# Performance work log

Hardware: AMD Instinct MI355X
Metric: run time of the kernel (lower is better)

Reference implementation:

```python
import jax, jax.numpy as jnp
import numpy as np

D_IN, D_OUT, H, L = 18, 2, 128, 2  # from load_pretrained config; bidirectional


def _uniform(key, shape, scale):
    return jax.random.uniform(key, shape, jnp.float32, -scale, scale)


def setup_inputs() -> dict:
    key = jax.random.key(0)
    ks = jax.random.split(key, 32)
    B, T = 64, 2048
    s = 1.0 / np.sqrt(H)
    inp = {"x": jax.random.normal(ks[0], (B, T, D_IN), jnp.float32)}
    i = 1
    for l in range(L):
        d_in_l = D_IN if l == 0 else 2 * H
        for suf in ("", "r"):
            inp[f"w_ih_l{l}{suf}"] = _uniform(ks[i], (3 * H, d_in_l), s); i += 1
            inp[f"w_hh_l{l}{suf}"] = _uniform(ks[i], (3 * H, H), s); i += 1
            inp[f"b_ih_l{l}{suf}"] = _uniform(ks[i], (3 * H,), s); i += 1
            inp[f"b_hh_l{l}{suf}"] = _uniform(ks[i], (3 * H,), s); i += 1
    inp["fc_w"] = _uniform(ks[i], (D_OUT, 2 * H), 1.0 / np.sqrt(2 * H)); i += 1
    inp["fc_b"] = _uniform(ks[i], (D_OUT,), 1.0 / np.sqrt(2 * H))
    return inp


def gru_dir(x, w_ih, w_hh, b_ih, b_hh, reverse):
    # x: [B,T,Din] -> [B,T,H], PyTorch GRU gate math (r,z,n ordering)
    B, T, _ = x.shape
    xg = jnp.einsum('btd,gd->btg', x, w_ih) + b_ih  # [B,T,3H], batched GEMM once
    if reverse:
        xg = xg[:, ::-1]
    def step(h, xt):
        gh = h @ w_hh.T + b_hh
        xr, xz, xn = jnp.split(xt, 3, axis=-1)
        hr, hz, hn = jnp.split(gh, 3, axis=-1)
        r = jax.nn.sigmoid(xr + hr)
        z = jax.nn.sigmoid(xz + hz)
        n = jnp.tanh(xn + r * hn)
        h_new = (1.0 - z) * n + z * h
        return h_new, h_new
    h0 = jnp.zeros((B, H), x.dtype)
    _, ys = jax.lax.scan(step, h0, jnp.swapaxes(xg, 0, 1))  # scan over time
    ys = jnp.swapaxes(ys, 0, 1)
    if reverse:
        ys = ys[:, ::-1]
    return ys


def gru_forward(x, params):
    h = x
    for l in range(L):
        fwd = gru_dir(h, params[f"w_ih_l{l}"], params[f"w_hh_l{l}"],
                      params[f"b_ih_l{l}"], params[f"b_hh_l{l}"], False)
        bwd = gru_dir(h, params[f"w_ih_l{l}r"], params[f"w_hh_l{l}r"],
                      params[f"b_ih_l{l}r"], params[f"b_hh_l{l}r"], True)
        h = jnp.concatenate([fwd, bwd], axis=-1)  # [B,T,2H]; dropout off (eval)
    return h


def reference(x, w_ih_l0, w_hh_l0, b_ih_l0, b_hh_l0,
              w_ih_l0r, w_hh_l0r, b_ih_l0r, b_hh_l0r,
              w_ih_l1, w_hh_l1, b_ih_l1, b_hh_l1,
              w_ih_l1r, w_hh_l1r, b_ih_l1r, b_hh_l1r,
              fc_w, fc_b):
    params = dict(w_ih_l0=w_ih_l0, w_hh_l0=w_hh_l0, b_ih_l0=b_ih_l0, b_hh_l0=b_hh_l0,
                  w_ih_l0r=w_ih_l0r, w_hh_l0r=w_hh_l0r, b_ih_l0r=b_ih_l0r, b_hh_l0r=b_hh_l0r,
                  w_ih_l1=w_ih_l1, w_hh_l1=w_hh_l1, b_ih_l1=b_ih_l1, b_hh_l1=b_hh_l1,
                  w_ih_l1r=w_ih_l1r, w_hh_l1r=w_hh_l1r, b_ih_l1r=b_ih_l1r, b_hh_l1r=b_hh_l1r)
    h = gru_forward(x, params)
    return jnp.einsum('bth,oh->bto', h, fc_w) + fc_b  # [B,T,D_OUT]
```

## Files before the change

kernel.cpp:

```cpp
#include <hip/hip_runtime.h>
#include <hip/hip_bf16.h>

#define B_   64
#define T_   2048
#define H_   128
#define G_   384
#define D0_  18
#define WIN  4
#define RING 8
#define NW   (T_ / WIN)

typedef __hip_bfloat16 bf16;
typedef __attribute__((ext_vector_type(4))) float f32x4;
typedef __attribute__((ext_vector_type(8))) short s16x8;

#define LOG2E  1.4426950408889634f
#define NEGL2E (-1.4426950408889634f)
#define TWOL2E (2.8853900817779268f)

__device__ __forceinline__ short f2bs(float v) {
    bf16 b = __float2bfloat16(v);
    return *reinterpret_cast<short*>(&b);
}
__device__ __forceinline__ unsigned short f2bu(float v) {
    bf16 b = __float2bfloat16(v);
    return *reinterpret_cast<unsigned short*>(&b);
}
__device__ __forceinline__ uint2 pk_bf16x4(float a, float b, float c, float d) {
    uint2 r;
    asm("v_cvt_pk_bf16_f32 %0, %1, %2" : "=v"(r.x) : "v"(a), "v"(b));
    asm("v_cvt_pk_bf16_f32 %0, %1, %2" : "=v"(r.y) : "v"(c), "v"(d));
    return r;
}
#define MFMA16(A, B, C) __builtin_amdgcn_mfma_f32_16x16x32_bf16((A), (B), (C), 0, 0, 0)

__device__ __forceinline__ void step_sync() {
    __asm__ volatile("s_waitcnt lgkmcnt(0)" ::: "memory");
    __builtin_amdgcn_s_barrier();
    __asm__ volatile("" ::: "memory");
}

__device__ __forceinline__ float gru_update(float yr, float yz, float aN,
                                            float aX, float h) {
    const float Er = __builtin_amdgcn_exp2f(yr);
    const float rg = __builtin_amdgcn_rcpf(1.0f + Er);
    const float En = __builtin_amdgcn_exp2f(fmaf(rg, aN, aX));
    const float Ez = __builtin_amdgcn_exp2f(yz);
    const float p  = fmaf(En, Ez, -Ez);
    const float q2 = fmaf(h, En, h);
    const float t1 = Ez + 1.0f;
    const float dn = fmaf(En, t1, t1);
    return (p + q2) * __builtin_amdgcn_rcpf(dn);
}


__global__ __launch_bounds__(512) void gru_l0_mfma(
    const float* __restrict__ x,
    const float* __restrict__ wih_f, const float* __restrict__ whh_f,
    const float* __restrict__ bih_f, const float* __restrict__ bhh_f,
    const float* __restrict__ wih_r, const float* __restrict__ whh_r,
    const float* __restrict__ bih_r, const float* __restrict__ bhh_r,
    bf16* __restrict__ l0h)
{
    __shared__ __align__(16) bf16 hring[RING][2048];
    __shared__ __align__(16) bf16 xbuf[2][WIN][512];

    const int bx   = blockIdx.x;
    const int dir  = bx >> 2;
    const int bg   = bx & 3;
    const int b0   = bg * 16;
    const int tid  = threadIdx.x;
    const int lane = tid & 63;
    const int wv   = tid >> 6;
    const int col  = lane & 15;
    const int quad = lane >> 4;

    const float* Wih = dir ? wih_r : wih_f;
    const float* Whh = dir ? whh_r : whh_f;
    const float* Bih = dir ? bih_r : bih_f;
    const float* Bhh = dir ? bhh_r : bhh_f;

    const float GSC[3] = {NEGL2E, NEGL2E, TWOL2E};

    s16x8 wfr[3][4], wxf[3];
    #pragma unroll
    for (int g = 0; g < 3; ++g) {
        const float sc = GSC[g];
        const float* wrow = Whh + (size_t)(g * H_ + wv * 16 + col) * H_;
        #pragma unroll
        for (int kt = 0; kt < 4; ++kt) {
            const float* p = wrow + kt * 32 + quad * 8;
            s16x8 f;
            #pragma unroll
            for (int i = 0; i < 8; ++i) f[i] = f2bs(p[i] * sc);
            wfr[g][kt] = f;
        }
        const float* xrow = Wih + (size_t)(g * H_ + wv * 16 + col) * D0_;
        s16x8 fx;
        #pragma unroll
        for (int i = 0; i < 8; ++i) {
            const int k = quad * 8 + i;
            fx[i] = (k < D0_) ? f2bs(xrow[k] * sc) : (short)0;
        }
        wxf[g] = fx;
    }
    f32x4 sR, sZ, sX, sN;
    #pragma unroll
    for (int r = 0; r < 4; ++r) {
        const int j = wv * 16 + quad * 4 + r;
        sR[r] = (Bih[j]        + Bhh[j])      * NEGL2E;
        sZ[r] = (Bih[H_ + j]   + Bhh[H_ + j]) * NEGL2E;
        sX[r] = Bih[2*H_ + j]  * TWOL2E;
        sN[r] = Bhh[2*H_ + j]  * TWOL2E;
    }

    const int wkt   = wv >> 1;
    const int wl    = (((wv << 1) + (quad >> 1)) & 3) * 16 + col;
    const int woff  = wkt * 512 + wl * 8 + (quad & 1) * 4;

    for (int i = tid; i < 2048; i += 512) hring[0][i] = __float2bfloat16(0.0f);
    #pragma unroll
    for (int k = 0; k < 4; ++k) {
        const int i = tid + k * 512;
        const int si = i >> 9, rem = i & 511;
        const int m = (rem >> 5) & 15, c = rem & 31;
        const int t = dir ? (T_ - 1 - si) : si;
        const float v = (c < D0_) ? x[((size_t)(b0 + m) * T_ + t) * D0_ + c] : 0.0f;
        xbuf[0][si][((c >> 3) * 16 + m) * 8 + (c & 7)] = __float2bfloat16(v);
    }
    __syncthreads();

    float hprev[4] = {0.f, 0.f, 0.f, 0.f};
    float xv[4];

    for (int w = 0; w < NW; ++w) {
        const int par = w & 1;
        s16x8 axf[WIN];
        #pragma unroll
        for (int si = 0; si < WIN; ++si)
            axf[si] = *(const s16x8*)&xbuf[par][si][lane * 8];

        #pragma unroll
        for (int si = 0; si < WIN; ++si) {
            const int s  = w * WIN + si;
            const int rb = s & (RING - 1);
            const int wb = (s + 1) & (RING - 1);

            s16x8 hfr[4];
            #pragma unroll
            for (int kt = 0; kt < 4; ++kt)
                hfr[kt] = *(const s16x8*)&hring[rb][kt * 512 + lane * 8];

            f32x4 aR = MFMA16(wxf[0], axf[si], sR);
            f32x4 aZ = MFMA16(wxf[1], axf[si], sZ);
            f32x4 aX = MFMA16(wxf[2], axf[si], sX);
            f32x4 aN = sN;
            #pragma unroll
            for (int kt = 0; kt < 4; ++kt) {
                aR = MFMA16(wfr[0][kt], hfr[kt], aR);
                aZ = MFMA16(wfr[1][kt], hfr[kt], aZ);
                aN = MFMA16(wfr[2][kt], hfr[kt], aN);
            }

            if (si == 1 && w > 0) {
                #pragma unroll
                for (int k = 0; k < 2; ++k) {
                    const int c  = tid + k * 512;
                    const int dt = c >> 8, m = (c >> 4) & 15, jo = c & 15;
                    const int fs = (w - 1) * WIN + dt;
                    const int t  = dir ? (T_ - 1 - fs) : fs;
                    const uint4 v = *(const uint4*)
                        &hring[(fs + 1) & (RING - 1)][(jo >> 2) * 512 + ((jo & 3) * 16 + m) * 8];
                    *(uint4*)(l0h + ((size_t)(b0 + m) * T_ + t) * 256 + dir * H_ + jo * 8) = v;
                }
            }

            if (si == 0 && w + 1 < NW) {
                #pragma unroll
                for (int k = 0; k < 4; ++k) {
                    const int i = tid + k * 512;
                    const int sj = i >> 9, rem = i & 511;
                    const int m = (rem >> 5) & 15, c = rem & 31;
                    const int s2 = (w + 1) * WIN + sj;
                    const int t2 = dir ? (T_ - 1 - s2) : s2;
                    xv[k] = (c < D0_) ? x[((size_t)(b0 + m) * T_ + t2) * D0_ + c] : 0.0f;
                }
            }

            float hn4[4];
            #pragma unroll
            for (int r = 0; r < 4; ++r) {
                const float hn = gru_update(aR[r], aZ[r], aN[r], aX[r], hprev[r]);
                hprev[r] = hn;
                hn4[r] = hn;
            }
            *(uint2*)&hring[wb][woff] = pk_bf16x4(hn4[0], hn4[1], hn4[2], hn4[3]);

            if (si == 3 && w + 1 < NW) {
                #pragma unroll
                for (int k = 0; k < 4; ++k) {
                    const int i = tid + k * 512;
                    const int sj = i >> 9, rem = i & 511;
                    const int m = (rem >> 5) & 15, c = rem & 31;
                    xbuf[par ^ 1][sj][((c >> 3) * 16 + m) * 8 + (c & 7)] =
                        __float2bfloat16(xv[k]);
                }
            }
            step_sync();
        }
    }
    #pragma unroll
    for (int k = 0; k < 2; ++k) {
        const int c  = tid + k * 512;
        const int dt = c >> 8, m = (c >> 4) & 15, jo = c & 15;
        const int fs = (NW - 1) * WIN + dt;
        const int t  = dir ? (T_ - 1 - fs) : fs;
        const uint4 v = *(const uint4*)
            &hring[(fs + 1) & (RING - 1)][(jo >> 2) * 512 + ((jo & 3) * 16 + m) * 8];
        *(uint4*)(l0h + ((size_t)(b0 + m) * T_ + t) * 256 + dir * H_ + jo * 8) = v;
    }
}

__global__ __launch_bounds__(256, 2) void xg_gemm_mfma(
    const bf16* __restrict__ A,
    const float* __restrict__ w_f, const float* __restrict__ w_r,
    const float* __restrict__ bi_f, const float* __restrict__ bi_r,
    const float* __restrict__ bh_f, const float* __restrict__ bh_r,
    bf16* __restrict__ xg_f, bf16* __restrict__ xg_r)
{
    __shared__ short As[128 * 40];
    __shared__ short Ws[128 * 40];
    __shared__ float Bias_s[128];

    const int dir  = blockIdx.z;
    const float* W   = dir ? w_r : w_f;
    const float* bi  = dir ? bi_r : bi_f;
    const float* bh  = dir ? bh_r : bh_f;
    bf16* xg         = dir ? xg_r : xg_f;

    const int tid  = threadIdx.x;
    const int lane = tid & 63;
    const int wv   = tid >> 6;
    const int col  = lane & 15;
    const int quad = lane >> 4;
    const int n0   = blockIdx.x * 128;
    const int g    = blockIdx.y;
    const int m0   = g * 128;

    const float sc = (g < 2) ? NEGL2E : TWOL2E;

    if (tid < 128) {
        const int n = m0 + tid;
        Bias_s[tid] = (bi[n] + ((n < 2 * H_) ? bh[n] : 0.0f)) * sc;
    }

    f32x4 acc[2][8];
    #pragma unroll
    for (int mt = 0; mt < 2; ++mt)
        #pragma unroll
        for (int nt = 0; nt < 8; ++nt) acc[mt][nt] = (f32x4){0.f, 0.f, 0.f, 0.f};

    for (int k0 = 0; k0 < 256; k0 += 32) {
        #pragma unroll
        for (int i = 0; i < 2; ++i) {
            const int c = tid + i * 256;
            const int row = c >> 2, q4 = c & 3;
            *(uint4*)&As[row * 40 + q4 * 8] =
                *(const uint4*)(A + (size_t)(n0 + row) * 256 + k0 + q4 * 8);
        }
        #pragma unroll
        for (int i = 0; i < 4; ++i) {
            const int c = tid + i * 256;
            const int row = c >> 3, q = c & 7;
            const float4 v = *(const float4*)(W + (size_t)(m0 + row) * 256 + k0 + q * 4);
            ushort4 u;
            u.x = f2bu(v.x * sc); u.y = f2bu(v.y * sc);
            u.z = f2bu(v.z * sc); u.w = f2bu(v.w * sc);
            *(ushort4*)&Ws[row * 40 + q * 4] = u;
        }
        __syncthreads();

        s16x8 wfr[2], hfr[8];
        #pragma unroll
        for (int mt = 0; mt < 2; ++mt)
            wfr[mt] = *(const s16x8*)&Ws[(wv * 32 + mt * 16 + col) * 40 + quad * 8];
        #pragma unroll
        for (int nt = 0; nt < 8; ++nt)
            hfr[nt] = *(const s16x8*)&As[(nt * 16 + col) * 40 + quad * 8];

        #pragma unroll
        for (int mt = 0; mt < 2; ++mt)
            #pragma unroll
            for (int nt = 0; nt < 8; ++nt)
                acc[mt][nt] = MFMA16(wfr[mt], hfr[nt], acc[mt][nt]);
        __syncthreads();
    }

    const int batch = n0 >> 11;
    const int bg = batch >> 4, cm = batch & 15;
    #pragma unroll
    for (int mt = 0; mt < 2; ++mt) {
        const int jt = wv * 2 + mt;
        float bv[4];
        #pragma unroll
        for (int r = 0; r < 4; ++r)
            bv[r] = Bias_s[wv * 32 + mt * 16 + quad * 4 + r];
        #pragma unroll
        for (int nt = 0; nt < 8; ++nt) {
            const int t = (n0 & 2047) + nt * 16 + col;
            uint2 o;
            o.x = (unsigned)f2bu(acc[mt][nt][0] + bv[0]) |
                  ((unsigned)f2bu(acc[mt][nt][1] + bv[1]) << 16);
            o.y = (unsigned)f2bu(acc[mt][nt][2] + bv[2]) |
                  ((unsigned)f2bu(acc[mt][nt][3] + bv[3]) << 16);
            const size_t idx = ((((size_t)bg * T_ + t) * 3 + g) * 8 + jt) * 64
                             + quad * 16 + cm;
            ((uint2*)xg)[idx] = o;
        }
    }
}

__global__ __launch_bounds__(512) void gru_l1_mfma(
    const bf16* __restrict__ xg_f, const bf16* __restrict__ xg_r,
    const float* __restrict__ whh_f, const float* __restrict__ bhh_f,
    const float* __restrict__ whh_r, const float* __restrict__ bhh_r,
    bf16* __restrict__ l1h, int fixed_dir)
{
    __shared__ __align__(16) bf16 hring[RING][2048];

    const int bx   = blockIdx.x;
    const int dir  = (fixed_dir >= 0) ? fixed_dir : (bx >> 2);
    const int bg   = bx & 3;
    const int b0   = bg * 16;
    const int tid  = threadIdx.x;
    const int lane = tid & 63;
    const int wv   = tid >> 6;
    const int col  = lane & 15;
    const int quad = lane >> 4;

    const bf16*  XG  = dir ? xg_r : xg_f;
    const float* Whh = dir ? whh_r : whh_f;
    const float* Bhh = dir ? bhh_r : bhh_f;

    const float GSC[3] = {NEGL2E, NEGL2E, TWOL2E};

    s16x8 wfr[3][4];
    #pragma unroll
    for (int g = 0; g < 3; ++g) {
        const float sc = GSC[g];
        const float* wrow = Whh + (size_t)(g * H_ + wv * 16 + col) * H_;
        #pragma unroll
        for (int kt = 0; kt < 4; ++kt) {
            const float* p = wrow + kt * 32 + quad * 8;
            s16x8 f;
            #pragma unroll
            for (int i = 0; i < 8; ++i) f[i] = f2bs(p[i] * sc);
            wfr[g][kt] = f;
        }
    }
    f32x4 sN;
    #pragma unroll
    for (int r = 0; r < 4; ++r)
        sN[r] = Bhh[2*H_ + wv * 16 + quad * 4 + r] * TWOL2E;

    const int wkt  = wv >> 1;
    const int wl   = (((wv << 1) + (quad >> 1)) & 3) * 16 + col;
    const int woff = wkt * 512 + wl * 8 + (quad & 1) * 4;

    for (int i = tid; i < 2048; i += 512) hring[0][i] = __float2bfloat16(0.0f);

    const uint2* xgb = (const uint2*)XG + ((size_t)bg * T_) * 3 * 8 * 64;
    const int lidx = wv * 64 + lane;

    uint2 xcur[WIN][3], xnxt[WIN][3];
    #pragma unroll
    for (int si = 0; si < WIN; ++si) {
        const int t = dir ? (T_ - 1 - si) : si;
        #pragma unroll
        for (int g = 0; g < 3; ++g)
            xcur[si][g] = xgb[((size_t)t * 3 + g) * 512 + lidx];
    }
    __syncthreads();

    float hprev[4] = {0.f, 0.f, 0.f, 0.f};

    for (int w = 0; w < NW; ++w) {
        #pragma unroll
        for (int si = 0; si < WIN; ++si) {
            const int s  = w * WIN + si;
            const int rb = s & (RING - 1);
            const int wb = (s + 1) & (RING - 1);

            s16x8 hfr[4];
            #pragma unroll
            for (int kt = 0; kt < 4; ++kt)
                hfr[kt] = *(const s16x8*)&hring[rb][kt * 512 + lane * 8];

            const uint2 xr2 = xcur[si][0], xz2 = xcur[si][1], xn2 = xcur[si][2];
            const f32x4 seedR = (f32x4){
                __uint_as_float(xr2.x << 16), __uint_as_float(xr2.x & 0xffff0000u),
                __uint_as_float(xr2.y << 16), __uint_as_float(xr2.y & 0xffff0000u)};
            const f32x4 seedZ = (f32x4){
                __uint_as_float(xz2.x << 16), __uint_as_float(xz2.x & 0xffff0000u),
                __uint_as_float(xz2.y << 16), __uint_as_float(xz2.y & 0xffff0000u)};
            const float xnf[4] = {
                __uint_as_float(xn2.x << 16), __uint_as_float(xn2.x & 0xffff0000u),
                __uint_as_float(xn2.y << 16), __uint_as_float(xn2.y & 0xffff0000u)};

            f32x4 aR = seedR, aZ = seedZ, aN = sN;
            #pragma unroll
            for (int kt = 0; kt < 4; ++kt) {
                aR = MFMA16(wfr[0][kt], hfr[kt], aR);
                aZ = MFMA16(wfr[1][kt], hfr[kt], aZ);
                aN = MFMA16(wfr[2][kt], hfr[kt], aN);
            }

            if (si == 1 && w > 0) {
                #pragma unroll
                for (int k = 0; k < 2; ++k) {
                    const int c  = tid + k * 512;
                    const int dt = c >> 8, m = (c >> 4) & 15, jo = c & 15;
                    const int fs = (w - 1) * WIN + dt;
                    const int t  = dir ? (T_ - 1 - fs) : fs;
                    const uint4 v = *(const uint4*)
                        &hring[(fs + 1) & (RING - 1)][(jo >> 2) * 512 + ((jo & 3) * 16 + m) * 8];
                    *(uint4*)(l1h + ((size_t)(b0 + m) * T_ + t) * 256 + dir * H_ + jo * 8) = v;
                }
            }

            if (si == 0 && w + 1 < NW) {
                #pragma unroll
                for (int sj = 0; sj < WIN; ++sj) {
                    const int s2 = (w + 1) * WIN + sj;
                    const int t2 = dir ? (T_ - 1 - s2) : s2;
                    #pragma unroll
                    for (int g = 0; g < 3; ++g)
                        xnxt[sj][g] = xgb[((size_t)t2 * 3 + g) * 512 + lidx];
                }
            }

            float hn4[4];
            #pragma unroll
            for (int r = 0; r < 4; ++r) {
                const float hn = gru_update(aR[r], aZ[r], aN[r], xnf[r], hprev[r]);
                hprev[r] = hn;
                hn4[r] = hn;
            }
            *(uint2*)&hring[wb][woff] = pk_bf16x4(hn4[0], hn4[1], hn4[2], hn4[3]);

            step_sync();
        }

        #pragma unroll
        for (int si = 0; si < WIN; ++si) {
            xcur[si][0] = xnxt[si][0];
            xcur[si][1] = xnxt[si][1];
            xcur[si][2] = xnxt[si][2];
        }
    }
    #pragma unroll
    for (int k = 0; k < 2; ++k) {
        const int c  = tid + k * 512;
        const int dt = c >> 8, m = (c >> 4) & 15, jo = c & 15;
        const int fs = (NW - 1) * WIN + dt;
        const int t  = dir ? (T_ - 1 - fs) : fs;
        const uint4 v = *(const uint4*)
            &hring[(fs + 1) & (RING - 1)][(jo >> 2) * 512 + ((jo & 3) * 16 + m) * 8];
        *(uint4*)(l1h + ((size_t)(b0 + m) * T_ + t) * 256 + dir * H_ + jo * 8) = v;
    }
}

__global__ __launch_bounds__(256, 2) void fc_kernel(
    const bf16* __restrict__ h, const float* __restrict__ fcw,
    const float* __restrict__ fcb, float* __restrict__ out)
{
    __shared__ float w0[256], w1[256];
    const int tid = threadIdx.x;
    w0[tid] = fcw[tid];
    w1[tid] = fcw[256 + tid];
    __syncthreads();

    const size_t bt = (size_t)blockIdx.x * 256 + tid;
    const bf16* hp = h + bt * 256;
    float s0 = fcb[0], s1 = fcb[1];
    #pragma unroll 4
    for (int k8 = 0; k8 < 32; ++k8) {
        const uint4 u = *(const uint4*)(hp + k8 * 8);
        const unsigned uu[4] = {u.x, u.y, u.z, u.w};
        #pragma unroll
        for (int p = 0; p < 4; ++p) {
            const float v0 = __uint_as_float(uu[p] << 16);
            const float v1 = __uint_as_float(uu[p] & 0xffff0000u);
            const int k = k8 * 8 + p * 2;
            s0 = fmaf(w0[k], v0, s0);     s1 = fmaf(w1[k], v0, s1);
            s0 = fmaf(w0[k + 1], v1, s0); s1 = fmaf(w1[k + 1], v1, s1);
        }
    }
    out[bt * 2]     = s0;
    out[bt * 2 + 1] = s1;
}

extern "C" void kernel_launch(void* const* d_in, const int* in_sizes, int n_in,
                              void* d_out, int out_size, void* d_ws, size_t ws_size,
                              hipStream_t stream)
{
    if (n_in < 19) return;
    const float* x     = (const float*)d_in[0];
    const float* wih0  = (const float*)d_in[1];
    const float* whh0  = (const float*)d_in[2];
    const float* bih0  = (const float*)d_in[3];
    const float* bhh0  = (const float*)d_in[4];
    const float* wih0r = (const float*)d_in[5];
    const float* whh0r = (const float*)d_in[6];
    const float* bih0r = (const float*)d_in[7];
    const float* bhh0r = (const float*)d_in[8];
    const float* wih1  = (const float*)d_in[9];
    const float* whh1  = (const float*)d_in[10];
    const float* bih1  = (const float*)d_in[11];
    const float* bhh1  = (const float*)d_in[12];
    const float* wih1r = (const float*)d_in[13];
    const float* whh1r = (const float*)d_in[14];
    const float* bih1r = (const float*)d_in[15];
    const float* bhh1r = (const float*)d_in[16];
    const float* fcw   = (const float*)d_in[17];
    const float* fcb   = (const float*)d_in[18];
    float* out = (float*)d_out;

    const size_t nBT  = (size_t)B_ * T_;
    const size_t hh_b = nBT * 2 * H_ * sizeof(bf16);
    const size_t xg_b = nBT * G_ * sizeof(bf16);
    const size_t xg_el = nBT * G_;

    if (ws_size >= hh_b + 2 * xg_b) {
        bf16* l0h = (bf16*)d_ws;
        bf16* xgf = (bf16*)((char*)d_ws + hh_b);
        bf16* xgr = xgf + xg_el;

        gru_l0_mfma<<<dim3(8), dim3(512), 0, stream>>>(
            x, wih0, whh0, bih0, bhh0, wih0r, whh0r, bih0r, bhh0r, l0h);
        xg_gemm_mfma<<<dim3(1024, 3, 2), dim3(256), 0, stream>>>(
            l0h, wih1, wih1r, bih1, bih1r, bhh1, bhh1r, xgf, xgr);
        gru_l1_mfma<<<dim3(8), dim3(512), 0, stream>>>(
            xgf, xgr, whh1, bhh1, whh1r, bhh1r, l0h, -1);
        fc_kernel<<<dim3((int)(nBT / 256)), dim3(256), 0, stream>>>(l0h, fcw, fcb, out);
    } else if (ws_size >= 2 * hh_b + xg_b) {
        bf16* l0h = (bf16*)d_ws;
        bf16* xg  = (bf16*)((char*)d_ws + hh_b);
        bf16* l1h = (bf16*)((char*)d_ws + hh_b + xg_b);

        gru_l0_mfma<<<dim3(8), dim3(512), 0, stream>>>(
            x, wih0, whh0, bih0, bhh0, wih0r, whh0r, bih0r, bhh0r, l0h);
        xg_gemm_mfma<<<dim3(1024, 3, 1), dim3(256), 0, stream>>>(
            l0h, wih1, wih1, bih1, bih1, bhh1, bhh1, xg, xg);
        gru_l1_mfma<<<dim3(4), dim3(512), 0, stream>>>(
            xg, xg, whh1, bhh1, whh1r, bhh1r, l1h, 0);
        xg_gemm_mfma<<<dim3(1024, 3, 1), dim3(256), 0, stream>>>(
            l0h, wih1r, wih1r, bih1r, bih1r, bhh1r, bhh1r, xg, xg);
        gru_l1_mfma<<<dim3(4), dim3(512), 0, stream>>>(
            xg, xg, whh1, bhh1, whh1r, bhh1r, l1h, 1);
        fc_kernel<<<dim3((int)(nBT / 256)), dim3(256), 0, stream>>>(l1h, fcw, fcb, out);
    }
}
```

Baseline: 2.592 ms.

## Precompute layer-0 input gates with a GEMM and reuse the layer-1 recurrence kernel

Removes the dedicated layer-0 recurrent kernel, which did the small x·W_ih projection with MFMAs inside the serial time loop. A new parallel GEMM kernel now precomputes the layer-0 input gate pre-activations into the xg buffer, and the existing layer-1 recurrent kernel is reused for layer 0. This takes the x loading and input-projection MFMAs off the latency-critical sequential path. The cost is an extra kernel launch plus a write and read of the xg buffer through global memory.

```diff
diff --git a/kernel.cpp b/kernel.cpp
--- a/kernel.cpp
+++ b/kernel.cpp
@@ -53,272 +53,6 @@
     return (p + q2) * __builtin_amdgcn_rcpf(dn);
 }
 
-
-__global__ __launch_bounds__(512) void gru_l0_mfma(
-    const float* __restrict__ x,
-    const float* __restrict__ wih_f, const float* __restrict__ whh_f,
-    const float* __restrict__ bih_f, const float* __restrict__ bhh_f,
-    const float* __restrict__ wih_r, const float* __restrict__ whh_r,
-    const float* __restrict__ bih_r, const float* __restrict__ bhh_r,
-    bf16* __restrict__ l0h)
-{
-    __shared__ __align__(16) bf16 hring[RING][2048];
-    __shared__ __align__(16) bf16 xbuf[2][WIN][512];
-
-    const int bx   = blockIdx.x;
-    const int dir  = bx >> 2;
-    const int bg   = bx & 3;
-    const int b0   = bg * 16;
-    const int tid  = threadIdx.x;
-    const int lane = tid & 63;
-    const int wv   = tid >> 6;
-    const int col  = lane & 15;
-    const int quad = lane >> 4;
-
-    const float* Wih = dir ? wih_r : wih_f;
-    const float* Whh = dir ? whh_r : whh_f;
-    const float* Bih = dir ? bih_r : bih_f;
-    const float* Bhh = dir ? bhh_r : bhh_f;
-
-    const float GSC[3] = {NEGL2E, NEGL2E, TWOL2E};
-
-    s16x8 wfr[3][4], wxf[3];
-    #pragma unroll
-    for (int g = 0; g < 3; ++g) {
-        const float sc = GSC[g];
-        const float* wrow = Whh + (size_t)(g * H_ + wv * 16 + col) * H_;
-        #pragma unroll
-        for (int kt = 0; kt < 4; ++kt) {
-            const float* p = wrow + kt * 32 + quad * 8;
-            s16x8 f;
-            #pragma unroll
-            for (int i = 0; i < 8; ++i) f[i] = f2bs(p[i] * sc);
-            wfr[g][kt] = f;
-        }
-        const float* xrow = Wih + (size_t)(g * H_ + wv * 16 + col) * D0_;
-        s16x8 fx;
-        #pragma unroll
-        for (int i = 0; i < 8; ++i) {
-            const int k = quad * 8 + i;
-            fx[i] = (k < D0_) ? f2bs(xrow[k] * sc) : (short)0;
-        }
-        wxf[g] = fx;
-    }
-    f32x4 sR, sZ, sX, sN;
-    #pragma unroll
-    for (int r = 0; r < 4; ++r) {
-        const int j = wv * 16 + quad * 4 + r;
-        sR[r] = (Bih[j]        + Bhh[j])      * NEGL2E;
-        sZ[r] = (Bih[H_ + j]   + Bhh[H_ + j]) * NEGL2E;
-        sX[r] = Bih[2*H_ + j]  * TWOL2E;
-        sN[r] = Bhh[2*H_ + j]  * TWOL2E;
-    }
-
-    const int wkt   = wv >> 1;
-    const int wl    = (((wv << 1) + (quad >> 1)) & 3) * 16 + col;
-    const int woff  = wkt * 512 + wl * 8 + (quad & 1) * 4;
-
-    for (int i = tid; i < 2048; i += 512) hring[0][i] = __float2bfloat16(0.0f);
-    #pragma unroll
-    for (int k = 0; k < 4; ++k) {
-        const int i = tid + k * 512;
-        const int si = i >> 9, rem = i & 511;
-        const int m = (rem >> 5) & 15, c = rem & 31;
-        const int t = dir ? (T_ - 1 - si) : si;
-        const float v = (c < D0_) ? x[((size_t)(b0 + m) * T_ + t) * D0_ + c] : 0.0f;
-        xbuf[0][si][((c >> 3) * 16 + m) * 8 + (c & 7)] = __float2bfloat16(v);
-    }
-    __syncthreads();
-
-    float hprev[4] = {0.f, 0.f, 0.f, 0.f};
-    float xv[4];
-
-    for (int w = 0; w < NW; ++w) {
-        const int par = w & 1;
-        s16x8 axf[WIN];
-        #pragma unroll
-        for (int si = 0; si < WIN; ++si)
-            axf[si] = *(const s16x8*)&xbuf[par][si][lane * 8];
-
-        #pragma unroll
-        for (int si = 0; si < WIN; ++si) {
-            const int s  = w * WIN + si;
-            const int rb = s & (RING - 1);
-            const int wb = (s + 1) & (RING - 1);
-
-            s16x8 hfr[4];
-            #pragma unroll
-            for (int kt = 0; kt < 4; ++kt)
-                hfr[kt] = *(const s16x8*)&hring[rb][kt * 512 + lane * 8];
-
-            f32x4 aR = MFMA16(wxf[0], axf[si], sR);
-            f32x4 aZ = MFMA16(wxf[1], axf[si], sZ);
-            f32x4 aX = MFMA16(wxf[2], axf[si], sX);
-            f32x4 aN = sN;
-            #pragma unroll
-            for (int kt = 0; kt < 4; ++kt) {
-                aR = MFMA16(wfr[0][kt], hfr[kt], aR);
-                aZ = MFMA16(wfr[1][kt], hfr[kt], aZ);
-                aN = MFMA16(wfr[2][kt], hfr[kt], aN);
-            }
-
-            if (si == 1 && w > 0) {
-                #pragma unroll
-                for (int k = 0; k < 2; ++k) {
-                    const int c  = tid + k * 512;
-                    const int dt = c >> 8, m = (c >> 4) & 15, jo = c & 15;
-                    const int fs = (w - 1) * WIN + dt;
-                    const int t  = dir ? (T_ - 1 - fs) : fs;
-                    const uint4 v = *(const uint4*)
-                        &hring[(fs + 1) & (RING - 1)][(jo >> 2) * 512 + ((jo & 3) * 16 + m) * 8];
-                    *(uint4*)(l0h + ((size_t)(b0 + m) * T_ + t) * 256 + dir * H_ + jo * 8) = v;
-                }
-            }
-
-            if (si == 0 && w + 1 < NW) {
-                #pragma unroll
-                for (int k = 0; k < 4; ++k) {
-                    const int i = tid + k * 512;
-                    const int sj = i >> 9, rem = i & 511;
-                    const int m = (rem >> 5) & 15, c = rem & 31;
-                    const int s2 = (w + 1) * WIN + sj;
-                    const int t2 = dir ? (T_ - 1 - s2) : s2;
-                    xv[k] = (c < D0_) ? x[((size_t)(b0 + m) * T_ + t2) * D0_ + c] : 0.0f;
-                }
-            }
-
-            float hn4[4];
-            #pragma unroll
-            for (int r = 0; r < 4; ++r) {
-                const float hn = gru_update(aR[r], aZ[r], aN[r], aX[r], hprev[r]);
-                hprev[r] = hn;
-                hn4[r] = hn;
-            }
-            *(uint2*)&hring[wb][woff] = pk_bf16x4(hn4[0], hn4[1], hn4[2], hn4[3]);
-
-            if (si == 3 && w + 1 < NW) {
-                #pragma unroll
-                for (int k = 0; k < 4; ++k) {
-                    const int i = tid + k * 512;
-                    const int sj = i >> 9, rem = i & 511;
-                    const int m = (rem >> 5) & 15, c = rem & 31;
-                    xbuf[par ^ 1][sj][((c >> 3) * 16 + m) * 8 + (c & 7)] =
-                        __float2bfloat16(xv[k]);
-                }
-            }
-            step_sync();
-        }
-    }
-    #pragma unroll
-    for (int k = 0; k < 2; ++k) {
-        const int c  = tid + k * 512;
-        const int dt = c >> 8, m = (c >> 4) & 15, jo = c & 15;
-        const int fs = (NW - 1) * WIN + dt;
-        const int t  = dir ? (T_ - 1 - fs) : fs;
-        const uint4 v = *(const uint4*)
-            &hring[(fs + 1) & (RING - 1)][(jo >> 2) * 512 + ((jo & 3) * 16 + m) * 8];
-        *(uint4*)(l0h + ((size_t)(b0 + m) * T_ + t) * 256 + dir * H_ + jo * 8) = v;
-    }
-}
-
-__global__ __launch_bounds__(256, 2) void xg_gemm_mfma(
-    const bf16* __restrict__ A,
-    const float* __restrict__ w_f, const float* __restrict__ w_r,
-    const float* __restrict__ bi_f, const float* __restrict__ bi_r,
-    const float* __restrict__ bh_f, const float* __restrict__ bh_r,
-    bf16* __restrict__ xg_f, bf16* __restrict__ xg_r)
-{
-    __shared__ short As[128 * 40];
-    __shared__ short Ws[128 * 40];
-    __shared__ float Bias_s[128];
-
-    const int dir  = blockIdx.z;
-    const float* W   = dir ? w_r : w_f;
-    const float* bi  = dir ? bi_r : bi_f;
-    const float* bh  = dir ? bh_r : bh_f;
-    bf16* xg         = dir ? xg_r : xg_f;
-
-    const int tid  = threadIdx.x;
-    const int lane = tid & 63;
-    const int wv   = tid >> 6;
-    const int col  = lane & 15;
-    const int quad = lane >> 4;
-    const int n0   = blockIdx.x * 128;
-    const int g    = blockIdx.y;
-    const int m0   = g * 128;
-
-    const float sc = (g < 2) ? NEGL2E : TWOL2E;
-
-    if (tid < 128) {
-        const int n = m0 + tid;
-        Bias_s[tid] = (bi[n] + ((n < 2 * H_) ? bh[n] : 0.0f)) * sc;
-    }
-
-    f32x4 acc[2][8];
-    #pragma unroll
-    for (int mt = 0; mt < 2; ++mt)
-        #pragma unroll
-        for (int nt = 0; nt < 8; ++nt) acc[mt][nt] = (f32x4){0.f, 0.f, 0.f, 0.f};
-
-    for (int k0 = 0; k0 < 256; k0 += 32) {
-        #pragma unroll
-        for (int i = 0; i < 2; ++i) {
-            const int c = tid + i * 256;
-            const int row = c >> 2, q4 = c & 3;
-            *(uint4*)&As[row * 40 + q4 * 8] =
-                *(const uint4*)(A + (size_t)(n0 + row) * 256 + k0 + q4 * 8);
-        }
-        #pragma unroll
-        for (int i = 0; i < 4; ++i) {
-            const int c = tid + i * 256;
-            const int row = c >> 3, q = c & 7;
-            const float4 v = *(const float4*)(W + (size_t)(m0 + row) * 256 + k0 + q * 4);
-            ushort4 u;
-            u.x = f2bu(v.x * sc); u.y = f2bu(v.y * sc);
-            u.z = f2bu(v.z * sc); u.w = f2bu(v.w * sc);
-            *(ushort4*)&Ws[row * 40 + q * 4] = u;
-        }
-        __syncthreads();
-
-        s16x8 wfr[2], hfr[8];
-        #pragma unroll
-        for (int mt = 0; mt < 2; ++mt)
-            wfr[mt] = *(const s16x8*)&Ws[(wv * 32 + mt * 16 + col) * 40 + quad * 8];
-        #pragma unroll
-        for (int nt = 0; nt < 8; ++nt)
-            hfr[nt] = *(const s16x8*)&As[(nt * 16 + col) * 40 + quad * 8];
-
-        #pragma unroll
-        for (int mt = 0; mt < 2; ++mt)
-            #pragma unroll
-            for (int nt = 0; nt < 8; ++nt)
-                acc[mt][nt] = MFMA16(wfr[mt], hfr[nt], acc[mt][nt]);
-        __syncthreads();
-    }
-
-    const int batch = n0 >> 11;
-    const int bg = batch >> 4, cm = batch & 15;
-    #pragma unroll
-    for (int mt = 0; mt < 2; ++mt) {
-        const int jt = wv * 2 + mt;
-        float bv[4];
-        #pragma unroll
-        for (int r = 0; r < 4; ++r)
-            bv[r] = Bias_s[wv * 32 + mt * 16 + quad * 4 + r];
-        #pragma unroll
-        for (int nt = 0; nt < 8; ++nt) {
-            const int t = (n0 & 2047) + nt * 16 + col;
-            uint2 o;
-            o.x = (unsigned)f2bu(acc[mt][nt][0] + bv[0]) |
-                  ((unsigned)f2bu(acc[mt][nt][1] + bv[1]) << 16);
-            o.y = (unsigned)f2bu(acc[mt][nt][2] + bv[2]) |
-                  ((unsigned)f2bu(acc[mt][nt][3] + bv[3]) << 16);
-            const size_t idx = ((((size_t)bg * T_ + t) * 3 + g) * 8 + jt) * 64
-                             + quad * 16 + cm;
-            ((uint2*)xg)[idx] = o;
-        }
-    }
-}
 
 __global__ __launch_bounds__(512) void gru_l1_mfma(
     const bf16* __restrict__ xg_f, const bf16* __restrict__ xg_r,
@@ -467,6 +201,196 @@
         const uint4 v = *(const uint4*)
             &hring[(fs + 1) & (RING - 1)][(jo >> 2) * 512 + ((jo & 3) * 16 + m) * 8];
         *(uint4*)(l1h + ((size_t)(b0 + m) * T_ + t) * 256 + dir * H_ + jo * 8) = v;
+    }
+}
+
+__global__ __launch_bounds__(256, 2) void xg_gemm_mfma(
+    const bf16* __restrict__ A,
+    const float* __restrict__ w_f, const float* __restrict__ w_r,
+    const float* __restrict__ bi_f, const float* __restrict__ bi_r,
+    const float* __restrict__ bh_f, const float* __restrict__ bh_r,
+    bf16* __restrict__ xg_f, bf16* __restrict__ xg_r)
+{
+    __shared__ short As[128 * 40];
+    __shared__ short Ws[128 * 40];
+    __shared__ float Bias_s[128];
+
+    const int dir  = blockIdx.z;
+    const float* W   = dir ? w_r : w_f;
+    const float* bi  = dir ? bi_r : bi_f;
+    const float* bh  = dir ? bh_r : bh_f;
+    bf16* xg         = dir ? xg_r : xg_f;
+
+    const int tid  = threadIdx.x;
+    const int lane = tid & 63;
+    const int wv   = tid >> 6;
+    const int col  = lane & 15;
+    const int quad = lane >> 4;
+    const int n0   = blockIdx.x * 128;
+    const int g    = blockIdx.y;
+    const int m0   = g * 128;
+
+    const float sc = (g < 2) ? NEGL2E : TWOL2E;
+    const f32x4 z4 = {0.f, 0.f, 0.f, 0.f};
+
+    if (tid < 128) {
+        const int n = m0 + tid;
+        Bias_s[tid] = (bi[n] + ((n < 2 * H_) ? bh[n] : 0.0f)) * sc;
+    }
+
+    f32x4 acc[2][8];
+    #pragma unroll
+    for (int mt = 0; mt < 2; ++mt)
+        #pragma unroll
+        for (int nt = 0; nt < 8; ++nt) acc[mt][nt] = z4;
+
+    for (int k0 = 0; k0 < 256; k0 += 32) {
+        #pragma unroll
+        for (int i = 0; i < 2; ++i) {
+            const int c = tid + i * 256;
+            const int row = c >> 2, q4 = c & 3;
+            *(uint4*)&As[row * 40 + q4 * 8] =
+                *(const uint4*)(A + (size_t)(n0 + row) * 256 + k0 + q4 * 8);
+        }
+        #pragma unroll
+        for (int i = 0; i < 4; ++i) {
+            const int c = tid + i * 256;
+            const int row = c >> 3, q = c & 7;
+            const float4 v = *(const float4*)(W + (size_t)(m0 + row) * 256 + k0 + q * 4);
+            ushort4 u;
+            u.x = f2bu(v.x * sc); u.y = f2bu(v.y * sc);
+            u.z = f2bu(v.z * sc); u.w = f2bu(v.w * sc);
+            *(ushort4*)&Ws[row * 40 + q * 4] = u;
+        }
+        __syncthreads();
+
+        s16x8 wfr[2], hfr[8];
+        #pragma unroll
+        for (int mt = 0; mt < 2; ++mt)
+            wfr[mt] = *(const s16x8*)&Ws[(wv * 32 + mt * 16 + col) * 40 + quad * 8];
+        #pragma unroll
+        for (int nt = 0; nt < 8; ++nt)
+            hfr[nt] = *(const s16x8*)&As[(nt * 16 + col) * 40 + quad * 8];
+
+        #pragma unroll
+        for (int mt = 0; mt < 2; ++mt)
+            #pragma unroll
+            for (int nt = 0; nt < 8; ++nt)
+                acc[mt][nt] = MFMA16(wfr[mt], hfr[nt], acc[mt][nt]);
+        __syncthreads();
+    }
+
+    const int batch = n0 >> 11;
+    const int bg = batch >> 4, cm = batch & 15;
+    #pragma unroll
+    for (int mt = 0; mt < 2; ++mt) {
+        const int jt = wv * 2 + mt;
+        float bv[4];
+        #pragma unroll
+        for (int r = 0; r < 4; ++r)
+            bv[r] = Bias_s[wv * 32 + mt * 16 + quad * 4 + r];
+        #pragma unroll
+        for (int nt = 0; nt < 8; ++nt) {
+            const int t = (n0 & 2047) + nt * 16 + col;
+            uint2 o;
+            o.x = (unsigned)f2bu(acc[mt][nt][0] + bv[0]) |
+                  ((unsigned)f2bu(acc[mt][nt][1] + bv[1]) << 16);
+            o.y = (unsigned)f2bu(acc[mt][nt][2] + bv[2]) |
+                  ((unsigned)f2bu(acc[mt][nt][3] + bv[3]) << 16);
+            const size_t idx = ((((size_t)bg * T_ + t) * 3 + g) * 8 + jt) * 64
+                             + quad * 16 + cm;
+            ((uint2*)xg)[idx] = o;
+        }
+    }
+}
+
+__global__ __launch_bounds__(256, 2) void xg0_gemm_mfma(
+    const float* __restrict__ x,
+    const float* __restrict__ w_f, const float* __restrict__ w_r,
+    const float* __restrict__ bi_f, const float* __restrict__ bi_r,
+    const float* __restrict__ bh_f, const float* __restrict__ bh_r,
+    bf16* __restrict__ xg_f, bf16* __restrict__ xg_r)
+{
+    __shared__ short As[128 * 40];
+    __shared__ short Ws[128 * 40];
+    __shared__ float Bias_s[128];
+
+    const int dir  = blockIdx.z;
+    const float* W   = dir ? w_r : w_f;
+    const float* bi  = dir ? bi_r : bi_f;
+    const float* bh  = dir ? bh_r : bh_f;
+    bf16* xg         = dir ? xg_r : xg_f;
+
+    const int tid  = threadIdx.x;
+    const int lane = tid & 63;
+    const int wv   = tid >> 6;
+    const int col  = lane & 15;
+    const int quad = lane >> 4;
+    const int n0   = blockIdx.x * 128;
+    const int g    = blockIdx.y;
+    const int m0   = g * 128;
+
+    const float sc = (g < 2) ? NEGL2E : TWOL2E;
+    const f32x4 z4 = {0.f, 0.f, 0.f, 0.f};
+
+    if (tid < 128) {
+        const int n = m0 + tid;
+        Bias_s[tid] = (bi[n] + ((n < 2 * H_) ? bh[n] : 0.0f)) * sc;
+    }
+
+    for (int i = tid; i < 128 * 40 / 2; i += 256) {
+        ((unsigned*)As)[i] = 0u;
+        ((unsigned*)Ws)[i] = 0u;
+    }
+    __syncthreads();
+
+    const float* xb = x + (size_t)n0 * D0_;
+    for (int i = tid; i < 128 * D0_; i += 256) {
+        const int row = i / D0_, k = i - row * D0_;
+        As[row * 40 + k] = f2bs(xb[i]);
+    }
+    for (int i = tid; i < 128 * D0_; i += 256) {
+        const int row = i / D0_, k = i - row * D0_;
+        Ws[row * 40 + k] = f2bs(W[(size_t)(m0 + row) * D0_ + k] * sc);
+    }
+    __syncthreads();
+
+    s16x8 wfr[2], hfr[8];
+    #pragma unroll
+    for (int mt = 0; mt < 2; ++mt)
+        wfr[mt] = *(const s16x8*)&Ws[(wv * 32 + mt * 16 + col) * 40 + quad * 8];
+    #pragma unroll
+    for (int nt = 0; nt < 8; ++nt)
+        hfr[nt] = *(const s16x8*)&As[(nt * 16 + col) * 40 + quad * 8];
+
+    f32x4 acc[2][8];
+    #pragma unroll
+    for (int mt = 0; mt < 2; ++mt)
+        #pragma unroll
+        for (int nt = 0; nt < 8; ++nt)
+            acc[mt][nt] = MFMA16(wfr[mt], hfr[nt], z4);
+
+    const int batch = n0 >> 11;
+    const int bg = batch >> 4, cm = batch & 15;
+    #pragma unroll
+    for (int mt = 0; mt < 2; ++mt) {
+        const int jt = wv * 2 + mt;
+        float bv[4];
+        #pragma unroll
+        for (int r = 0; r < 4; ++r)
+            bv[r] = Bias_s[wv * 32 + mt * 16 + quad * 4 + r];
+        #pragma unroll
+        for (int nt = 0; nt < 8; ++nt) {
+            const int t = (n0 & 2047) + nt * 16 + col;
+            uint2 o;
+            o.x = (unsigned)f2bu(acc[mt][nt][0] + bv[0]) |
+                  ((unsigned)f2bu(acc[mt][nt][1] + bv[1]) << 16);
+            o.y = (unsigned)f2bu(acc[mt][nt][2] + bv[2]) |
+                  ((unsigned)f2bu(acc[mt][nt][3] + bv[3]) << 16);
+            const size_t idx = ((((size_t)bg * T_ + t) * 3 + g) * 8 + jt) * 64
+                             + quad * 16 + cm;
+            ((uint2*)xg)[idx] = o;
+        }
     }
 }
 
@@ -536,8 +460,10 @@
         bf16* xgf = (bf16*)((char*)d_ws + hh_b);
         bf16* xgr = xgf + xg_el;
 
-        gru_l0_mfma<<<dim3(8), dim3(512), 0, stream>>>(
-            x, wih0, whh0, bih0, bhh0, wih0r, whh0r, bih0r, bhh0r, l0h);
+        xg0_gemm_mfma<<<dim3(1024, 3, 2), dim3(256), 0, stream>>>(
+            x, wih0, wih0r, bih0, bih0r, bhh0, bhh0r, xgf, xgr);
+        gru_l1_mfma<<<dim3(8), dim3(512), 0, stream>>>(
+            xgf, xgr, whh0, bhh0, whh0r, bhh0r, l0h, -1);
         xg_gemm_mfma<<<dim3(1024, 3, 2), dim3(256), 0, stream>>>(
             l0h, wih1, wih1r, bih1, bih1r, bhh1, bhh1r, xgf, xgr);
         gru_l1_mfma<<<dim3(8), dim3(512), 0, stream>>>(
@@ -548,8 +474,14 @@
         bf16* xg  = (bf16*)((char*)d_ws + hh_b);
         bf16* l1h = (bf16*)((char*)d_ws + hh_b + xg_b);
 
-        gru_l0_mfma<<<dim3(8), dim3(512), 0, stream>>>(
-            x, wih0, whh0, bih0, bhh0, wih0r, whh0r, bih0r, bhh0r, l0h);
+        xg0_gemm_mfma<<<dim3(1024, 3, 1), dim3(256), 0, stream>>>(
+            x, wih0, wih0, bih0, bih0, bhh0, bhh0, xg, xg);
+        gru_l1_mfma<<<dim3(4), dim3(512), 0, stream>>>(
+            xg, xg, whh0, bhh0, whh0r, bhh0r, l0h, 0);
+        xg0_gemm_mfma<<<dim3(1024, 3, 1), dim3(256), 0, stream>>>(
+            x, wih0r, wih0r, bih0r, bih0r, bhh0r, bhh0r, xg, xg);
+        gru_l1_mfma<<<dim3(4), dim3(512), 0, stream>>>(
+            xg, xg, whh0, bhh0, whh0r, bhh0r, l0h, 1);
         xg_gemm_mfma<<<dim3(1024, 3, 1), dim3(256), 0, stream>>>(
             l0h, wih1, wih1, bih1, bih1, bhh1, bhh1, xg, xg);
         gru_l1_mfma<<<dim3(4), dim3(512), 0, stream>>>(
```

After: 2.751 ms. 6.1% more time.

## Fuse layer-1 input projection into recurrent GRU kernel with LDS prefetch

Applied to the files above, without the earlier changes.

Removes the separate xg_gemm kernel and its large bf16 gate buffer. The layer-1 recurrent kernel now keeps W_ih fragments in registers and computes the input projection per timestep with extra MFMAs. The l0h rows are streamed into a 4-slot LDS ring three steps ahead via global_load_lds. This cuts a launch and the xg write/read traffic, but adds 24 MFMAs per step to the serial critical path of an 8-block kernel and raises register pressure.

```diff
diff --git a/kernel.cpp b/kernel.cpp
--- a/kernel.cpp
+++ b/kernel.cpp
@@ -38,6 +38,12 @@
     __asm__ volatile("s_waitcnt lgkmcnt(0)" ::: "memory");
     __builtin_amdgcn_s_barrier();
     __asm__ volatile("" ::: "memory");
+}
+
+__device__ __forceinline__ void gload_lds16(const bf16* g, bf16* l) {
+    __builtin_amdgcn_global_load_lds(
+        (const __attribute__((address_space(1))) unsigned*)(const void*)g,
+        (__attribute__((address_space(3))) unsigned*)(void*)l, 16, 0, 0);
 }
 
 __device__ __forceinline__ float gru_update(float yr, float yz, float aN,
@@ -221,115 +227,19 @@
     }
 }
 
-__global__ __launch_bounds__(256, 2) void xg_gemm_mfma(
-    const bf16* __restrict__ A,
-    const float* __restrict__ w_f, const float* __restrict__ w_r,
-    const float* __restrict__ bi_f, const float* __restrict__ bi_r,
-    const float* __restrict__ bh_f, const float* __restrict__ bh_r,
-    bf16* __restrict__ xg_f, bf16* __restrict__ xg_r)
-{
-    __shared__ short As[128 * 40];
-    __shared__ short Ws[128 * 40];
-    __shared__ float Bias_s[128];
-
-    const int dir  = blockIdx.z;
-    const float* W   = dir ? w_r : w_f;
-    const float* bi  = dir ? bi_r : bi_f;
-    const float* bh  = dir ? bh_r : bh_f;
-    bf16* xg         = dir ? xg_r : xg_f;
-
-    const int tid  = threadIdx.x;
-    const int lane = tid & 63;
-    const int wv   = tid >> 6;
-    const int col  = lane & 15;
-    const int quad = lane >> 4;
-    const int n0   = blockIdx.x * 128;
-    const int g    = blockIdx.y;
-    const int m0   = g * 128;
-
-    const float sc = (g < 2) ? NEGL2E : TWOL2E;
-
-    if (tid < 128) {
-        const int n = m0 + tid;
-        Bias_s[tid] = (bi[n] + ((n < 2 * H_) ? bh[n] : 0.0f)) * sc;
-    }
-
-    f32x4 acc[2][8];
-    #pragma unroll
-    for (int mt = 0; mt < 2; ++mt)
-        #pragma unroll
-        for (int nt = 0; nt < 8; ++nt) acc[mt][nt] = (f32x4){0.f, 0.f, 0.f, 0.f};
-
-    for (int k0 = 0; k0 < 256; k0 += 32) {
-        #pragma unroll
-        for (int i = 0; i < 2; ++i) {
-            const int c = tid + i * 256;
-            const int row = c >> 2, q4 = c & 3;
-            *(uint4*)&As[row * 40 + q4 * 8] =
-                *(const uint4*)(A + (size_t)(n0 + row) * 256 + k0 + q4 * 8);
-        }
-        #pragma unroll
-        for (int i = 0; i < 4; ++i) {
-            const int c = tid + i * 256;
-            const int row = c >> 3, q = c & 7;
-            const float4 v = *(const float4*)(W + (size_t)(m0 + row) * 256 + k0 + q * 4);
-            ushort4 u;
-            u.x = f2bu(v.x * sc); u.y = f2bu(v.y * sc);
-            u.z = f2bu(v.z * sc); u.w = f2bu(v.w * sc);
-            *(ushort4*)&Ws[row * 40 + q * 4] = u;
-        }
-        __syncthreads();
-
-        s16x8 wfr[2], hfr[8];
-        #pragma unroll
-        for (int mt = 0; mt < 2; ++mt)
-            wfr[mt] = *(const s16x8*)&Ws[(wv * 32 + mt * 16 + col) * 40 + quad * 8];
-        #pragma unroll
-        for (int nt = 0; nt < 8; ++nt)
-            hfr[nt] = *(const s16x8*)&As[(nt * 16 + col) * 40 + quad * 8];
-
-        #pragma unroll
-        for (int mt = 0; mt < 2; ++mt)
-            #pragma unroll
-            for (int nt = 0; nt < 8; ++nt)
-                acc[mt][nt] = MFMA16(wfr[mt], hfr[nt], acc[mt][nt]);
-        __syncthreads();
-    }
-
-    const int batch = n0 >> 11;
-    const int bg = batch >> 4, cm = batch & 15;
-    #pragma unroll
-    for (int mt = 0; mt < 2; ++mt) {
-        const int jt = wv * 2 + mt;
-        float bv[4];
-        #pragma unroll
-        for (int r = 0; r < 4; ++r)
-            bv[r] = Bias_s[wv * 32 + mt * 16 + quad * 4 + r];
-        #pragma unroll
-        for (int nt = 0; nt < 8; ++nt) {
-            const int t = (n0 & 2047) + nt * 16 + col;
-            uint2 o;
-            o.x = (unsigned)f2bu(acc[mt][nt][0] + bv[0]) |
-                  ((unsigned)f2bu(acc[mt][nt][1] + bv[1]) << 16);
-            o.y = (unsigned)f2bu(acc[mt][nt][2] + bv[2]) |
-                  ((unsigned)f2bu(acc[mt][nt][3] + bv[3]) << 16);
-            const size_t idx = ((((size_t)bg * T_ + t) * 3 + g) * 8 + jt) * 64
-                             + quad * 16 + cm;
-            ((uint2*)xg)[idx] = o;
-        }
-    }
-}
-
 __global__ __launch_bounds__(512) void gru_l1_mfma(
-    const bf16* __restrict__ xg_f, const bf16* __restrict__ xg_r,
-    const float* __restrict__ whh_f, const float* __restrict__ bhh_f,
-    const float* __restrict__ whh_r, const float* __restrict__ bhh_r,
-    bf16* __restrict__ l1h, int fixed_dir)
+    const bf16* __restrict__ l0h,
+    const float* __restrict__ wih_f, const float* __restrict__ whh_f,
+    const float* __restrict__ bih_f, const float* __restrict__ bhh_f,
+    const float* __restrict__ wih_r, const float* __restrict__ whh_r,
+    const float* __restrict__ bih_r, const float* __restrict__ bhh_r,
+    bf16* __restrict__ l1h)
 {
     __shared__ __align__(16) bf16 hring[RING][2048];
+    __shared__ __align__(16) bf16 xstage[4][4096];
 
     const int bx   = blockIdx.x;
-    const int dir  = (fixed_dir >= 0) ? fixed_dir : (bx >> 2);
+    const int dir  = bx >> 2;
     const int bg   = bx & 3;
     const int b0   = bg * 16;
     const int tid  = threadIdx.x;
@@ -338,8 +248,9 @@
     const int col  = lane & 15;
     const int quad = lane >> 4;
 
-    const bf16*  XG  = dir ? xg_r : xg_f;
+    const float* Wih = dir ? wih_r : wih_f;
     const float* Whh = dir ? whh_r : whh_f;
+    const float* Bih = dir ? bih_r : bih_f;
     const float* Bhh = dir ? bhh_r : bhh_f;
 
     const float GSC[3] = {NEGL2E, NEGL2E, TWOL2E};
@@ -358,10 +269,29 @@
             wfr[g][kt] = f;
         }
     }
-    f32x4 sN;
-    #pragma unroll
-    for (int r = 0; r < 4; ++r)
-        sN[r] = Bhh[2*H_ + wv * 16 + quad * 4 + r] * TWOL2E;
+    s16x8 wxf[3][8];
+    #pragma unroll
+    for (int g = 0; g < 3; ++g) {
+        const float sc = GSC[g];
+        const float* wrow = Wih + (size_t)(g * H_ + wv * 16 + col) * 256;
+        #pragma unroll
+        for (int k2 = 0; k2 < 8; ++k2) {
+            const float* p = wrow + k2 * 32 + quad * 8;
+            s16x8 f;
+            #pragma unroll
+            for (int i = 0; i < 8; ++i) f[i] = f2bs(p[i] * sc);
+            wxf[g][k2] = f;
+        }
+    }
+    f32x4 sR, sZ, sX, sN;
+    #pragma unroll
+    for (int r = 0; r < 4; ++r) {
+        const int j = wv * 16 + quad * 4 + r;
+        sR[r] = (Bih[j]        + Bhh[j])      * NEGL2E;
+        sZ[r] = (Bih[H_ + j]   + Bhh[H_ + j]) * NEGL2E;
+        sX[r] = Bih[2*H_ + j]  * TWOL2E;
+        sN[r] = Bhh[2*H_ + j]  * TWOL2E;
+    }
 
     const int wkt  = wv >> 1;
     const int wl   = (((wv << 1) + (quad >> 1)) & 3) * 16 + col;
@@ -369,17 +299,16 @@
 
     for (int i = tid; i < 2048; i += 512) hring[0][i] = __float2bfloat16(0.0f);
 
-    const uint2* xgb = (const uint2*)XG + ((size_t)bg * T_) * 3 * 8 * 64;
-    const int lidx = wv * 64 + lane;
-
-    uint2 xcur[WIN][3], xnxt[WIN][3];
-    #pragma unroll
-    for (int si = 0; si < WIN; ++si) {
-        const int t = dir ? (T_ - 1 - si) : si;
-        #pragma unroll
-        for (int g = 0; g < 3; ++g)
-            xcur[si][g] = xgb[((size_t)t * 3 + g) * 512 + lidx];
-    }
+    const bf16* xp = l0h + ((size_t)(b0 + (lane & 15)) * T_ + (dir ? T_ - 1 : 0)) * 256
+                   + wv * 32 + quad * 8;
+    const ptrdiff_t xstep = dir ? -256 : 256;
+
+    #pragma unroll
+    for (int s = 0; s < 3; ++s) {
+        gload_lds16(xp, &xstage[s][wv * 512]);
+        xp += xstep;
+    }
+    __asm__ volatile("s_waitcnt vmcnt(0)" ::: "memory");
     __syncthreads();
 
     float hprev[4] = {0.f, 0.f, 0.f, 0.f};
@@ -390,24 +319,29 @@
             const int s  = w * WIN + si;
             const int rb = s & (RING - 1);
             const int wb = (s + 1) & (RING - 1);
+            const int xb = s & 3;
 
             s16x8 hfr[4];
             #pragma unroll
             for (int kt = 0; kt < 4; ++kt)
                 hfr[kt] = *(const s16x8*)&hring[rb][kt * 512 + lane * 8];
-
-            const uint2 xr2 = xcur[si][0], xz2 = xcur[si][1], xn2 = xcur[si][2];
-            const f32x4 seedR = (f32x4){
-                __uint_as_float(xr2.x << 16), __uint_as_float(xr2.x & 0xffff0000u),
-                __uint_as_float(xr2.y << 16), __uint_as_float(xr2.y & 0xffff0000u)};
-            const f32x4 seedZ = (f32x4){
-                __uint_as_float(xz2.x << 16), __uint_as_float(xz2.x & 0xffff0000u),
-                __uint_as_float(xz2.y << 16), __uint_as_float(xz2.y & 0xffff0000u)};
-            const float xnf[4] = {
-                __uint_as_float(xn2.x << 16), __uint_as_float(xn2.x & 0xffff0000u),
-                __uint_as_float(xn2.y << 16), __uint_as_float(xn2.y & 0xffff0000u)};
-
-            f32x4 aR = seedR, aZ = seedZ, aN = sN;
+            s16x8 xfr[8];
+            #pragma unroll
+            for (int k2 = 0; k2 < 8; ++k2)
+                xfr[k2] = *(const s16x8*)&xstage[xb][k2 * 512 + lane * 8];
+
+            if (s + 3 < T_) {
+                gload_lds16(xp, &xstage[(s + 3) & 3][wv * 512]);
+                xp += xstep;
+            }
+
+            f32x4 aR = sR, aZ = sZ, aX = sX, aN = sN;
+            #pragma unroll
+            for (int k2 = 0; k2 < 8; ++k2) {
+                aR = MFMA16(wxf[0][k2], xfr[k2], aR);
+                aZ = MFMA16(wxf[1][k2], xfr[k2], aZ);
+                aX = MFMA16(wxf[2][k2], xfr[k2], aX);
+            }
             #pragma unroll
             for (int kt = 0; kt < 4; ++kt) {
                 aR = MFMA16(wfr[0][kt], hfr[kt], aR);
@@ -428,34 +362,17 @@
                 }
             }
 
-            if (si == 0 && w + 1 < NW) {
-                #pragma unroll
-                for (int sj = 0; sj < WIN; ++sj) {
-                    const int s2 = (w + 1) * WIN + sj;
-                    const int t2 = dir ? (T_ - 1 - s2) : s2;
-                    #pragma unroll
-                    for (int g = 0; g < 3; ++g)
-                        xnxt[sj][g] = xgb[((size_t)t2 * 3 + g) * 512 + lidx];
-                }
-            }
-
             float hn4[4];
             #pragma unroll
             for (int r = 0; r < 4; ++r) {
-                const float hn = gru_update(aR[r], aZ[r], aN[r], xnf[r], hprev[r]);
+                const float hn = gru_update(aR[r], aZ[r], aN[r], aX[r], hprev[r]);
                 hprev[r] = hn;
                 hn4[r] = hn;
             }
             *(uint2*)&hring[wb][woff] = pk_bf16x4(hn4[0], hn4[1], hn4[2], hn4[3]);
 
+            __asm__ volatile("s_waitcnt vmcnt(4)" ::: "memory");
             step_sync();
-        }
-
-        #pragma unroll
-        for (int si = 0; si < WIN; ++si) {
-            xcur[si][0] = xnxt[si][0];
-            xcur[si][1] = xnxt[si][1];
-            xcur[si][2] = xnxt[si][2];
         }
     }
     #pragma unroll
@@ -528,36 +445,15 @@
 
     const size_t nBT  = (size_t)B_ * T_;
     const size_t hh_b = nBT * 2 * H_ * sizeof(bf16);
-    const size_t xg_b = nBT * G_ * sizeof(bf16);
-    const size_t xg_el = nBT * G_;
-
-    if (ws_size >= hh_b + 2 * xg_b) {
+
+    if (ws_size >= 2 * hh_b) {
         bf16* l0h = (bf16*)d_ws;
-        bf16* xgf = (bf16*)((char*)d_ws + hh_b);
-        bf16* xgr = xgf + xg_el;
+        bf16* l1h = (bf16*)((char*)d_ws + hh_b);
 
         gru_l0_mfma<<<dim3(8), dim3(512), 0, stream>>>(
             x, wih0, whh0, bih0, bhh0, wih0r, whh0r, bih0r, bhh0r, l0h);
-        xg_gemm_mfma<<<dim3(1024, 3, 2), dim3(256), 0, stream>>>(
-            l0h, wih1, wih1r, bih1, bih1r, bhh1, bhh1r, xgf, xgr);
         gru_l1_mfma<<<dim3(8), dim3(512), 0, stream>>>(
-            xgf, xgr, whh1, bhh1, whh1r, bhh1r, l0h, -1);
-        fc_kernel<<<dim3((int)(nBT / 256)), dim3(256), 0, stream>>>(l0h, fcw, fcb, out);
-    } else if (ws_size >= 2 * hh_b + xg_b) {
-        bf16* l0h = (bf16*)d_ws;
-        bf16* xg  = (bf16*)((char*)d_ws + hh_b);
-        bf16* l1h = (bf16*)((char*)d_ws + hh_b + xg_b);
-
-        gru_l0_mfma<<<dim3(8), dim3(512), 0, stream>>>(
-            x, wih0, whh0, bih0, bhh0, wih0r, whh0r, bih0r, bhh0r, l0h);
-        xg_gemm_mfma<<<dim3(1024, 3, 1), dim3(256), 0, stream>>>(
-            l0h, wih1, wih1, bih1, bih1, bhh1, bhh1, xg, xg);
-        gru_l1_mfma<<<dim3(4), dim3(512), 0, stream>>>(
-            xg, xg, whh1, bhh1, whh1r, bhh1r, l1h, 0);
-        xg_gemm_mfma<<<dim3(1024, 3, 1), dim3(256), 0, stream>>>(
-            l0h, wih1r, wih1r, bih1r, bih1r, bhh1r, bhh1r, xg, xg);
-        gru_l1_mfma<<<dim3(4), dim3(512), 0, stream>>>(
-            xg, xg, whh1, bhh1, whh1r, bhh1r, l1h, 1);
+            l0h, wih1, whh1, bih1, bhh1, wih1r, whh1r, bih1r, bhh1r, l1h);
         fc_kernel<<<dim3((int)(nBT / 256)), dim3(256), 0, stream>>>(l1h, fcw, fcb, out);
     }
 }
```

After: 3.175 ms. +22.5%, slower.
